# Kernel optimization log

Hardware: AMD Instinct MI355X
Metric: run time of the kernel (lower is better)

## Reference

```python
import jax, jax.numpy as jnp
import numpy as np

D_MODEL = 2048
NUM_HEADS = 16
N_KV_HEADS = 4
HEAD_DIM = D_MODEL // NUM_HEADS  # 128
N_REP = NUM_HEADS // N_KV_HEADS  # 4
WINDOW = 256
ROPE_BASE = 10000.0
B, T = 2, 2048


def setup_inputs() -> dict:
    key = jax.random.key(0)
    ks = jax.random.split(key, 5)
    s_in = 1.0 / np.sqrt(D_MODEL)
    return {
        "x": jax.random.normal(ks[0], (B, T, D_MODEL), jnp.float32),
        "Wq": jax.random.normal(ks[1], (D_MODEL, D_MODEL), jnp.float32) * s_in,
        "Wk": jax.random.normal(ks[2], (D_MODEL, N_KV_HEADS * HEAD_DIM), jnp.float32) * s_in,
        "Wv": jax.random.normal(ks[3], (D_MODEL, N_KV_HEADS * HEAD_DIM), jnp.float32) * s_in,
        "Wo": jax.random.normal(ks[4], (D_MODEL, D_MODEL), jnp.float32) * s_in,
    }


def _rope_tables(seqlen, dtype):
    inv_freq = 1.0 / (ROPE_BASE ** (jnp.arange(0, HEAD_DIM, 2, dtype=jnp.float32) / HEAD_DIM))
    t = jnp.arange(seqlen, dtype=jnp.float32)
    freqs = jnp.outer(t, inv_freq)              # [T, hd/2]
    emb = jnp.concatenate([freqs, freqs], -1)   # [T, hd]
    return jnp.cos(emb).astype(dtype), jnp.sin(emb).astype(dtype)


def _rotate_half(x):
    half = x.shape[-1] // 2
    return jnp.concatenate([-x[..., half:], x[..., :half]], -1)


def reference(x, Wq, Wk, Wv, Wo):
    Bb, Tt, _ = x.shape
    q = (x @ Wq).reshape(Bb, Tt, NUM_HEADS, HEAD_DIM).transpose(0, 2, 1, 3)   # [B,H,T,hd]
    k = (x @ Wk).reshape(Bb, Tt, N_KV_HEADS, HEAD_DIM).transpose(0, 2, 1, 3)  # [B,Hkv,T,hd]
    v = (x @ Wv).reshape(Bb, Tt, N_KV_HEADS, HEAD_DIM).transpose(0, 2, 1, 3)

    cos, sin = _rope_tables(Tt, q.dtype)  # [T, hd] each, broadcast over B,H
    q = q * cos + _rotate_half(q) * sin
    k = k * cos + _rotate_half(k) * sin

    # GQA: repeat kv heads to match query heads
    k = jnp.repeat(k, N_REP, axis=1)
    v = jnp.repeat(v, N_REP, axis=1)

    # banded causal sliding-window mask: 0 <= i - j < WINDOW
    rel = jnp.arange(Tt)[:, None] - jnp.arange(Tt)[None, :]
    allowed = (rel >= 0) & (rel < WINDOW)  # [T, T]

    scale = 1.0 / np.sqrt(HEAD_DIM)
    scores = jnp.einsum('bhqd,bhkd->bhqk', q, k) * scale
    scores = jnp.where(allowed, scores, jnp.finfo(scores.dtype).min)
    probs = jax.nn.softmax(scores, axis=-1)
    y = jnp.einsum('bhqk,bhkd->bhqd', probs, v)
    y = y.transpose(0, 2, 1, 3).reshape(Bb, Tt, D_MODEL)
    return y @ Wo
```

## Files before the change

### kernel.cpp

```cpp
#include <hip/hip_runtime.h>
#include <hip/hip_bf16.h>

#define D_MODEL 2048
#define SEQ_T   2048
#define NQH     16
#define NKVH    4
#define HD      128
#define WIN     256
#define BATCH   2
#define ROWS    (BATCH * SEQ_T)
#define L2_10K  13.287712379549449f
#define GK      2048

typedef __attribute__((ext_vector_type(8))) short bf8_t;
typedef __attribute__((ext_vector_type(4))) float f4_t;

__device__ __forceinline__ float bf2f(unsigned short u) {
    union { unsigned int i; float f; } v; v.i = ((unsigned int)u) << 16; return v.f;
}
__device__ __forceinline__ unsigned short f2bf(float f) {
    union { float f; unsigned int i; } v; v.f = f;
    unsigned int x = v.i;
    unsigned int lsb = (x >> 16) & 1u;
    x += 0x7fffu + lsb;
    return (unsigned short)(x >> 16);
}

__device__ __forceinline__ void async_ld16(const unsigned short* g, unsigned short* l) {
    __builtin_amdgcn_global_load_lds(
        (const __attribute__((address_space(1))) unsigned int*)(g),
        (__attribute__((address_space(3))) unsigned int*)(l), 16, 0, 0);
}

__device__ int sniff_is_f32(const unsigned short* p) {
    int sane = 0;
    for (int i = 0; i < 64; ++i) {
        unsigned short u = p[2 * i];
        int e = (u >> 7) & 0xFF;
        sane += (e >= 100 && e <= 140) ? 1 : 0;
    }
    return sane < 32;
}

__global__ __launch_bounds__(256)
void convert_all(const float* __restrict__ x,
                 const float* __restrict__ Wq, const float* __restrict__ Wk,
                 const float* __restrict__ Wv, const float* __restrict__ Wo,
                 unsigned short* __restrict__ xb,
                 unsigned short* __restrict__ Wqkvt, unsigned short* __restrict__ Wot) {
    __shared__ unsigned short Ts[32][36];
    int id = blockIdx.x;
    const int t = threadIdx.x;
    if (id < 4096) {
        int i = (id * 256 + t) * 8;
        float4 a = *(const float4*)(x + i);
        float4 b = *(const float4*)(x + i + 4);
        ushort4 o0, o1;
        o0.x = f2bf(a.x); o0.y = f2bf(a.y); o0.z = f2bf(a.z); o0.w = f2bf(a.w);
        o1.x = f2bf(b.x); o1.y = f2bf(b.y); o1.z = f2bf(b.z); o1.w = f2bf(b.w);
        *(ushort4*)(xb + i)     = o0;
        *(ushort4*)(xb + i + 4) = o1;
        return;
    }
    id -= 4096;
    const float* W; unsigned short* Wt; int N;
    const int K = D_MODEL;
    if (id < 4096)      { W = Wq; Wt = Wqkvt;                          N = 2048; }
    else if (id < 5120) { W = Wk; Wt = Wqkvt + (size_t)2048 * D_MODEL; N = 512;  id -= 4096; }
    else if (id < 6144) { W = Wv; Wt = Wqkvt + (size_t)2560 * D_MODEL; N = 512;  id -= 5120; }
    else                { W = Wo; Wt = Wot;                            N = 2048; id -= 6144; }
    const int ntn = N >> 5;
    const int n0 = (id % ntn) * 32;
    const int k0 = (id / ntn) * 32;
    {
        int r = t >> 3, c = (t & 7) * 4;
        float4 v = *(const float4*)(W + (size_t)(k0 + r) * N + n0 + c);
        Ts[r][c + 0] = f2bf(v.x); Ts[r][c + 1] = f2bf(v.y);
        Ts[r][c + 2] = f2bf(v.z); Ts[r][c + 3] = f2bf(v.w);
    }
    __syncthreads();
    {
        int n = t >> 3, k = (t & 7) * 4;
        ushort4 o;
        o.x = Ts[k + 0][n]; o.y = Ts[k + 1][n];
        o.z = Ts[k + 2][n]; o.w = Ts[k + 3][n];
        *(ushort4*)(Wt + (size_t)(n0 + n) * K + k0 + k) = o;
    }
}

__global__ __launch_bounds__(256, 3)
void gemm128r(const unsigned short* __restrict__ A,
              const unsigned short* __restrict__ Bt,
              void* __restrict__ Cq, void* __restrict__ Ck, void* __restrict__ Cvc,
              int N, int mode) {
    __shared__ __align__(16) unsigned short Ls[3][8192];

    const int tid  = threadIdx.x;
    const int w    = tid >> 6;
    const int lane = tid & 63;
    const int quad = lane >> 4;
    const int lr   = lane & 15;
    const int wm   = w >> 1;
    const int wn   = w & 1;
    const int sl   = ((quad + (lr >> 1)) & 3) * 8;

    const int ntn = N >> 7;
    const int g   = blockIdx.x;
    const int xcd = g & 7;
    const int r   = g >> 3;
    const int bm  = (xcd & 3) * 8 + (r & 7);
    const int bn  = (xcd >> 2) * (ntn >> 1) + (r >> 3);
    const int m0  = bm * 128;
    const int n0  = bn * 128;

    const unsigned short* srcA[2];
    const unsigned short* srcB[2];
    int dchunk[2];
    #pragma unroll
    for (int l = 0; l < 2; ++l) {
        int li   = l * 256 + tid;
        int row  = li >> 2;
        int slog = ((li & 3) - ((li >> 3) & 3)) & 3;
        srcA[l]   = A  + (size_t)(m0 + row) * GK + slog * 8;
        srcB[l]   = Bt + (size_t)(n0 + row) * GK + slog * 8;
        dchunk[l] = (l * 256 + w * 64) * 8;
    }

    f4_t acc[4][4];
    #pragma unroll
    for (int i = 0; i < 4; ++i)
        #pragma unroll
        for (int j = 0; j < 4; ++j) acc[i][j] = (f4_t){0.f, 0.f, 0.f, 0.f};

#define STAGE(S, KT) do {                                           \
        const int ko_ = (KT) * 32;                                  \
        async_ld16(srcA[0] + ko_, &Ls[S][dchunk[0]]);               \
        async_ld16(srcA[1] + ko_, &Ls[S][dchunk[1]]);               \
        async_ld16(srcB[0] + ko_, &Ls[S][4096 + dchunk[0]]);        \
        async_ld16(srcB[1] + ko_, &Ls[S][4096 + dchunk[1]]);        \
    } while (0)

#define GATE(NN) asm volatile("s_waitcnt vmcnt(" #NN ")" ::: "memory")

    STAGE(0, 0); STAGE(1, 1);
    GATE(4);
    __builtin_amdgcn_s_barrier();

    int Sc = 0, Ss = 2;
    for (int t = 0; t < 64; ++t) {
        const unsigned short* LA = &Ls[Sc][0];
        const unsigned short* LB = &Ls[Sc][4096];
        bf8_t af[4], bv[4];
        #pragma unroll
        for (int mf = 0; mf < 4; ++mf)
            af[mf] = *(const bf8_t*)&LA[(wm * 64 + mf * 16 + lr) * 32 + sl];
        #pragma unroll
        for (int nf = 0; nf < 4; ++nf)
            bv[nf] = *(const bf8_t*)&LB[(wn * 16 + nf * 32 + lr) * 32 + sl];
        if (t < 62) STAGE(Ss, t + 2);
        __builtin_amdgcn_s_setprio(1);
        #pragma unroll
        for (int nf = 0; nf < 4; ++nf)
            #pragma unroll
            for (int mf = 0; mf < 4; ++mf)
                acc[mf][nf] = __builtin_amdgcn_mfma_f32_16x16x32_bf16(
                    af[mf], bv[nf], acc[mf][nf], 0, 0, 0);
        __builtin_amdgcn_s_setprio(0);
        if (t < 62)       GATE(4);
        else if (t == 62) GATE(0);
        if (t < 63) __builtin_amdgcn_s_barrier();
        Sc = (Sc == 2) ? 0 : Sc + 1;
        Ss = (Ss == 2) ? 0 : Ss + 1;
    }

#undef STAGE
#undef GATE

    if (mode == 1) {
        float* C = (float*)Cq;
        #pragma unroll
        for (int mf = 0; mf < 4; ++mf)
            #pragma unroll
            for (int nf = 0; nf < 4; ++nf) {
                int c  = n0 + wn * 16 + nf * 32 + lr;
                int rb = m0 + wm * 64 + mf * 16 + quad * 4;
                #pragma unroll
                for (int rr = 0; rr < 4; ++rr)
                    C[(size_t)(rb + rr) * N + c] = acc[mf][nf][rr];
            }
        return;
    }
    if (n0 < 2048 + 512) {
        const bool isQ = (n0 < 2048);
        unsigned short* Cb = isQ ? (unsigned short*)Cq : (unsigned short*)Ck;
        const int ldc = isQ ? D_MODEL : (NKVH * HD);
        const int cb0 = isQ ? n0 : (n0 - 2048);
        float inv[2];
        #pragma unroll
        for (int p = 0; p < 2; ++p)
            inv[p] = exp2f(-(float)(wn * 16 + p * 32 + lr) * (L2_10K / 64.0f));
        #pragma unroll
        for (int mf = 0; mf < 4; ++mf) {
            #pragma unroll
            for (int rr = 0; rr < 4; ++rr) {
                int row = m0 + wm * 64 + mf * 16 + quad * 4 + rr;
                float tp = (float)(row & (SEQ_T - 1));
                #pragma unroll
                for (int p = 0; p < 2; ++p) {
                    float sn, cs;
                    sincosf(tp * inv[p], &sn, &cs);
                    float lo = acc[mf][p][rr], hi = acc[mf][p + 2][rr];
                    size_t base = (size_t)row * ldc + cb0 + wn * 16 + p * 32 + lr;
                    Cb[base]      = f2bf(lo * cs - hi * sn);
                    Cb[base + 64] = f2bf(hi * cs + lo * sn);
                }
            }
        }
    } else {
        unsigned short* Vc = (unsigned short*)Cvc;
        #pragma unroll
        for (int mf = 0; mf < 4; ++mf)
            #pragma unroll
            for (int nf = 0; nf < 4; ++nf) {
                int n    = (n0 - 2560) + wn * 16 + nf * 32 + lr;
                int kvh2 = n >> 7, d = n & 127;
                int row0 = m0 + wm * 64 + mf * 16 + quad * 4;
                int bb   = row0 >> 11, pos = row0 & (SEQ_T - 1);
                ushort4 o;
                o.x = f2bf(acc[mf][nf][0]); o.y = f2bf(acc[mf][nf][1]);
                o.z = f2bf(acc[mf][nf][2]); o.w = f2bf(acc[mf][nf][3]);
                *(ushort4*)(Vc + (size_t)(bb * 4 + kvh2) * (SEQ_T * HD)
                              + (size_t)(pos >> 5) * 4096 + d * 32 + (pos & 31)) = o;
            }
    }
}

__global__ __launch_bounds__(512, 2)
void gemm128(const unsigned short* __restrict__ A,
             const unsigned short* __restrict__ Bt,
             float* __restrict__ C, int N) {
    __shared__ __align__(16) unsigned short Ls[4][12288];

    const int tid  = threadIdx.x;
    const int w    = tid >> 6;
    const int lane = tid & 63;
    const int quad = lane >> 4;
    const int lr   = lane & 15;
    const int wm   = w >> 2;
    const int wn   = w & 3;
    const int sl   = ((quad + (lr >> 1)) & 3) * 8;

    const int ntn = N >> 8;
    const int g   = blockIdx.x;
    const int xcd = g & 7;
    const int r   = g >> 3;
    const int bm  = (xcd & 3) * 8 + (r & 7);
    const int bn  = (xcd >> 2) * (ntn >> 1) + (r >> 3);
    const int m0  = bm * 128;
    const int n0  = bn * 256;

    const int slog = ((tid & 3) - ((tid >> 3) & 3)) & 3;
    const unsigned short* srcA0 = A  + (size_t)(m0 + (tid >> 2)) * GK + slog * 8;
    const unsigned short* srcB0 = Bt + (size_t)(n0 + (tid >> 2)) * GK + slog * 8;
    const unsigned short* srcB1 = Bt + (size_t)(n0 + 128 + (tid >> 2)) * GK + slog * 8;
    const int dch = w * 512;

    f4_t acc[4][4];
    #pragma unroll
    for (int i = 0; i < 4; ++i)
        #pragma unroll
        for (int j = 0; j < 4; ++j) acc[i][j] = (f4_t){0.f, 0.f, 0.f, 0.f};

#define STAGEB(S, KT) do {                                          \
        const int ko_ = (KT) * 32;                                  \
        async_ld16(srcA0 + ko_, &Ls[S][dch]);                       \
        async_ld16(srcB0 + ko_, &Ls[S][4096 + dch]);                \
        async_ld16(srcB1 + ko_, &Ls[S][8192 + dch]);                \
    } while (0)

#define GATE(NN) asm volatile("s_waitcnt vmcnt(" #NN ")" ::: "memory")

    STAGEB(0, 0); STAGEB(1, 1); STAGEB(2, 2);
    GATE(6);
    __builtin_amdgcn_s_barrier();

    bf8_t af[4], bv[4];
    for (int t = 0; t < 64; ++t) {
        const int S = t & 3;
        #pragma unroll
        for (int mf = 0; mf < 4; ++mf)
            af[mf] = *(const bf8_t*)&Ls[S][(wm * 64 + mf * 16 + lr) * 32 + sl];
        #pragma unroll
        for (int nf = 0; nf < 4; ++nf)
            bv[nf] = *(const bf8_t*)&Ls[S][4096 + (wn * 16 + nf * 64 + lr) * 32 + sl];
        if (t < 61) STAGEB((t + 3) & 3, t + 3);
        __builtin_amdgcn_s_barrier();
        __builtin_amdgcn_s_setprio(1);
        #pragma unroll
        for (int nf = 0; nf < 4; ++nf)
            #pragma unroll
            for (int mf = 0; mf < 4; ++mf)
                acc[mf][nf] = __builtin_amdgcn_mfma_f32_16x16x32_bf16(
                    af[mf], bv[nf], acc[mf][nf], 0, 0, 0);
        __builtin_amdgcn_s_setprio(0);
        if (t < 61)      GATE(6);
        else if (t == 61) GATE(3);
        else if (t == 62) GATE(0);
        if (t < 63) __builtin_amdgcn_s_barrier();
    }

#undef STAGEB
#undef GATE

    #pragma unroll
    for (int mf = 0; mf < 4; ++mf)
        #pragma unroll
        for (int nf = 0; nf < 4; ++nf) {
            int c  = n0 + wn * 16 + nf * 64 + lr;
            int rb = m0 + wm * 64 + mf * 16 + quad * 4;
            #pragma unroll
            for (int rr = 0; rr < 4; ++rr)
                C[(size_t)(rb + rr) * N + c] = acc[mf][nf][rr];
        }
}

__global__ __launch_bounds__(256)
void gemm_dual(const void* __restrict__ A, const void* __restrict__ B,
               void* __restrict__ C, int M, int N, int Kd,
               const unsigned short* __restrict__ sniffp,
               int a_dyn, int c_dyn, int c_trans) {
    __shared__ unsigned short As[64][32];
    __shared__ unsigned short Bs[64][32];
    __shared__ int s_f32;

    const int t = threadIdx.x;
    if (t == 0) s_f32 = sniff_is_f32(sniffp);

    const int m0 = blockIdx.y * 64, n0 = blockIdx.x * 64;
    const int w = t >> 6, lane = t & 63;
    const int wm = w >> 1, wn = w & 1;
    const int quad = lane >> 4, lr = lane & 15;

    f4_t acc[2][2];
    #pragma unroll
    for (int i = 0; i < 2; ++i)
        #pragma unroll
        for (int j = 0; j < 2; ++j)
            acc[i][j] = (f4_t){0.f, 0.f, 0.f, 0.f};

    const int ar = t >> 2, ac = (t & 3) * 8;
    const int bk = t >> 3, bn = (t & 7) * 8;

    __syncthreads();
    const bool in_f32 = (s_f32 != 0);
    const bool a_f32  = in_f32 && (a_dyn != 0);
    const bool c_f32  = in_f32 && (c_dyn != 0);

    for (int k0 = 0; k0 < Kd; k0 += 32) {
        __syncthreads();
        if (a_f32) {
            const float* Af = (const float*)A;
            const float4* pa = (const float4*)(Af + (size_t)(m0 + ar) * Kd + k0 + ac);
            float4 a0 = pa[0], a1 = pa[1];
            unsigned short* d = &As[ar][ac];
            d[0] = f2bf(a0.x); d[1] = f2bf(a0.y); d[2] = f2bf(a0.z); d[3] = f2bf(a0.w);
            d[4] = f2bf(a1.x); d[5] = f2bf(a1.y); d[6] = f2bf(a1.z); d[7] = f2bf(a1.w);
        } else {
            const unsigned short* Au = (const unsigned short*)A;
            *(uint4*)(&As[ar][ac]) = *(const uint4*)(Au + (size_t)(m0 + ar) * Kd + k0 + ac);
        }
        if (in_f32) {
            const float* Bf = (const float*)B;
            const float4* pb = (const float4*)(Bf + (size_t)(k0 + bk) * N + n0 + bn);
            float4 b0 = pb[0], b1 = pb[1];
            Bs[bn + 0][bk] = f2bf(b0.x); Bs[bn + 1][bk] = f2bf(b0.y);
            Bs[bn + 2][bk] = f2bf(b0.z); Bs[bn + 3][bk] = f2bf(b0.w);
            Bs[bn + 4][bk] = f2bf(b1.x); Bs[bn + 5][bk] = f2bf(b1.y);
            Bs[bn + 6][bk] = f2bf(b1.z); Bs[bn + 7][bk] = f2bf(b1.w);
        } else {
            const unsigned short* Bu = (const unsigned short*)B;
            uint4 bv = *(const uint4*)(Bu + (size_t)(k0 + bk) * N + n0 + bn);
            union { uint4 v; unsigned short s[8]; } bu; bu.v = bv;
            #pragma unroll
            for (int j = 0; j < 8; ++j) Bs[bn + j][bk] = bu.s[j];
        }
        __syncthreads();

        bf8_t va0 = *(const bf8_t*)&As[wm * 32 + 0  + lr][quad * 8];
        bf8_t va1 = *(const bf8_t*)&As[wm * 32 + 16 + lr][quad * 8];
        bf8_t vb0 = *(const bf8_t*)&Bs[wn * 32 + 0  + lr][quad * 8];
        bf8_t vb1 = *(const bf8_t*)&Bs[wn * 32 + 16 + lr][quad * 8];

        acc[0][0] = __builtin_amdgcn_mfma_f32_16x16x32_bf16(va0, vb0, acc[0][0], 0, 0, 0);
        acc[0][1] = __builtin_amdgcn_mfma_f32_16x16x32_bf16(va0, vb1, acc[0][1], 0, 0, 0);
        acc[1][0] = __builtin_amdgcn_mfma_f32_16x16x32_bf16(va1, vb0, acc[1][0], 0, 0, 0);
        acc[1][1] = __builtin_amdgcn_mfma_f32_16x16x32_bf16(va1, vb1, acc[1][1], 0, 0, 0);
    }

    if (c_trans) {
        #pragma unroll
        for (int mi = 0; mi < 2; ++mi)
            #pragma unroll
            for (int ni = 0; ni < 2; ++ni) {
                int row0 = m0 + wm * 32 + mi * 16 + quad * 4;
                int col  = n0 + wn * 32 + ni * 16 + lr;
                int kvh2 = col >> 7, d = col & 127;
                int bb   = row0 >> 11, pos = row0 & (SEQ_T - 1);
                ushort4 v;
                v.x = f2bf(acc[mi][ni][0]); v.y = f2bf(acc[mi][ni][1]);
                v.z = f2bf(acc[mi][ni][2]); v.w = f2bf(acc[mi][ni][3]);
                *(ushort4*)((unsigned short*)C + (size_t)(bb * 4 + kvh2) * (SEQ_T * HD)
                              + (size_t)(pos >> 5) * 4096 + d * 32 + (pos & 31)) = v;
            }
    } else {
        #pragma unroll
        for (int mi = 0; mi < 2; ++mi)
            #pragma unroll
            for (int ni = 0; ni < 2; ++ni)
                #pragma unroll
                for (int r = 0; r < 4; ++r) {
                    int row = m0 + wm * 32 + mi * 16 + quad * 4 + r;
                    int col = n0 + wn * 32 + ni * 16 + lr;
                    if (c_f32) ((float*)C)[(size_t)row * N + col] = acc[mi][ni][r];
                    else ((unsigned short*)C)[(size_t)row * N + col] = f2bf(acc[mi][ni][r]);
                }
    }
}

__global__ __launch_bounds__(64)
void rope_kernel(unsigned short* __restrict__ X, int nheads) {
    const int idx = blockIdx.x;
    const int h   = idx % nheads;
    const int row = idx / nheads;
    const int tpos = row % SEQ_T;
    const int i   = threadIdx.x;

    size_t base = (size_t)row * (nheads * HD) + h * HD;
    float inv = exp2f(-(float)i * (L2_10K / 64.0f));
    float a = (float)tpos * inv;
    float s, c;
    sincosf(a, &s, &c);
    float x0 = bf2f(X[base + i]);
    float x1 = bf2f(X[base + i + 64]);
    X[base + i]      = f2bf(x0 * c - x1 * s);
    X[base + i + 64] = f2bf(x1 * c + x0 * s);
}

#define PS  72

__global__ __launch_bounds__(64)
void attn_gqa(unsigned short* __restrict__ Q,
              const unsigned short* __restrict__ K,
              const unsigned short* __restrict__ Vc) {
    __shared__ unsigned short Pw[32][PS];

    const int t    = threadIdx.x;
    const int g    = blockIdx.x;
    const int xcd  = g & 7;
    const int b    = xcd >> 2;
    const int kvh  = xcd & 3;
    const int h4   = (g >> 3) & 3;
    const int q0   = (g >> 5) * 32;
    const int quad = t >> 4;
    const int lr   = t & 15;
    const int h    = kvh * 4 + h4;
    const float scale = 0.08838834764831845f;

    bf8_t qf[2][4];
    #pragma unroll
    for (int mt = 0; mt < 2; ++mt) {
        const unsigned short* qrow =
            Q + (size_t)(b * SEQ_T + q0 + mt * 16 + lr) * D_MODEL + h * HD;
        #pragma unroll
        for (int kk = 0; kk < 4; ++kk)
            qf[mt][kk] = *(const bf8_t*)(qrow + kk * 32 + quad * 8);
    }

    f4_t O[2][8];
    #pragma unroll
    for (int mt = 0; mt < 2; ++mt)
        #pragma unroll
        for (int dt = 0; dt < 8; ++dt) O[mt][dt] = (f4_t){0.f, 0.f, 0.f, 0.f};
    float lpart[2][4];
    #pragma unroll
    for (int mt = 0; mt < 2; ++mt)
        #pragma unroll
        for (int r = 0; r < 4; ++r) lpart[mt][r] = 0.f;

    const size_t vbase = (size_t)(b * 4 + kvh) * (SEQ_T * HD);
    const int jstart = (q0 >= 193) ? 0 : ((193 - q0 + 63) >> 6);

    for (int j = jstart; j < 5; ++j) {
        const int kb = q0 - 256 + 64 * j;
        const bool need_mask = (j == 0) || (j == 4) || (kb < 0);

        bf8_t kf[4][4];
        #pragma unroll
        for (int nt = 0; nt < 4; ++nt) {
            int rg = kb + nt * 16 + lr;
            rg = rg < 0 ? 0 : (rg > SEQ_T - 1 ? SEQ_T - 1 : rg);
            const unsigned short* kr =
                K + (size_t)(b * SEQ_T + rg) * (NKVH * HD) + kvh * HD;
            #pragma unroll
            for (int kk = 0; kk < 4; ++kk)
                kf[nt][kk] = *(const bf8_t*)(kr + kk * 32 + quad * 8);
        }

        f4_t s[2][4];
        #pragma unroll
        for (int mt = 0; mt < 2; ++mt)
            #pragma unroll
            for (int nt = 0; nt < 4; ++nt) s[mt][nt] = (f4_t){0.f, 0.f, 0.f, 0.f};
        #pragma unroll
        for (int nt = 0; nt < 4; ++nt)
            #pragma unroll
            for (int kk = 0; kk < 4; ++kk) {
                s[0][nt] = __builtin_amdgcn_mfma_f32_16x16x32_bf16(qf[0][kk], kf[nt][kk], s[0][nt], 0, 0, 0);
                s[1][nt] = __builtin_amdgcn_mfma_f32_16x16x32_bf16(qf[1][kk], kf[nt][kk], s[1][nt], 0, 0, 0);
            }

        bf8_t vf[2][8];
        #pragma unroll
        for (int kk = 0; kk < 2; ++kk) {
            int slb = (kb + kk * 32) >> 5;
            slb = slb < 0 ? 0 : (slb > 63 ? 63 : slb);
            const unsigned short* vbp = Vc + vbase + (size_t)slb * 4096 + quad * 8;
            #pragma unroll
            for (int dt = 0; dt < 8; ++dt)
                vf[kk][dt] = *(const bf8_t*)(vbp + (dt * 16 + lr) * 32);
        }

        #pragma unroll
        for (int mt = 0; mt < 2; ++mt)
            #pragma unroll
            for (int r = 0; r < 4; ++r) {
                const int q = q0 + mt * 16 + quad * 4 + r;
                #pragma unroll
                for (int nt = 0; nt < 4; ++nt) {
                    float pj = __expf(s[mt][nt][r] * scale);
                    if (need_mask) {
                        int jg = kb + nt * 16 + lr;
                        bool ok = (jg >= 0) && ((unsigned)(q - jg) < (unsigned)WIN);
                        pj = ok ? pj : 0.f;
                    }
                    lpart[mt][r] += pj;
                    Pw[mt * 16 + quad * 4 + r][nt * 16 + lr] = f2bf(pj);
                }
            }

        bf8_t pf[2][2];
        #pragma unroll
        for (int mt = 0; mt < 2; ++mt)
            #pragma unroll
            for (int kk = 0; kk < 2; ++kk)
                pf[mt][kk] = *(const bf8_t*)&Pw[mt * 16 + lr][kk * 32 + quad * 8];
        #pragma unroll
        for (int dt = 0; dt < 8; ++dt)
            #pragma unroll
            for (int kk = 0; kk < 2; ++kk) {
                O[0][dt] = __builtin_amdgcn_mfma_f32_16x16x32_bf16(pf[0][kk], vf[kk][dt], O[0][dt], 0, 0, 0);
                O[1][dt] = __builtin_amdgcn_mfma_f32_16x16x32_bf16(pf[1][kk], vf[kk][dt], O[1][dt], 0, 0, 0);
            }
    }

    #pragma unroll
    for (int off = 1; off < 16; off <<= 1)
        #pragma unroll
        for (int mt = 0; mt < 2; ++mt)
            #pragma unroll
            for (int r = 0; r < 4; ++r)
                lpart[mt][r] += __shfl_xor(lpart[mt][r], off);

    #pragma unroll
    for (int mt = 0; mt < 2; ++mt) {
        float invl[4];
        #pragma unroll
        for (int r = 0; r < 4; ++r) invl[r] = 1.0f / lpart[mt][r];
        #pragma unroll
        for (int dt = 0; dt < 8; ++dt)
            #pragma unroll
            for (int r = 0; r < 4; ++r)
                Q[(size_t)(b * SEQ_T + q0 + mt * 16 + quad * 4 + r) * D_MODEL
                  + h * HD + dt * 16 + lr] = f2bf(O[mt][dt][r] * invl[r]);
    }
}

extern "C" void kernel_launch(void* const* d_in, const int* in_sizes, int n_in,
                              void* d_out, int out_size, void* d_ws, size_t ws_size,
                              hipStream_t stream) {
    const float* x  = (const float*)d_in[0];
    const float* Wq = (const float*)d_in[1];
    const float* Wk = (const float*)d_in[2];
    const float* Wv = (const float*)d_in[3];
    const float* Wo = (const float*)d_in[4];
    const unsigned short* sniffp = (const unsigned short*)d_in[1];

    unsigned short* Qb  = (unsigned short*)d_ws;
    unsigned short* Kb  = Qb + (size_t)ROWS * D_MODEL;
    unsigned short* Vcb = Kb + (size_t)ROWS * (NKVH * HD);
    unsigned short* Wot = Vcb + (size_t)(NKVH * HD) * ROWS;

    dim3 blk(256);

    if (ws_size >= (size_t)32 * 1024 * 1024) {
        unsigned short* xb    = (unsigned short*)d_out;
        unsigned short* Wqkvt = xb + (size_t)ROWS * D_MODEL;

        convert_all<<<dim3(14336), blk, 0, stream>>>(x, Wq, Wk, Wv, Wo, xb, Wqkvt, Wot);

        gemm128r<<<dim3(768), blk, 0, stream>>>(
            xb, Wqkvt, Qb, Kb, Vcb, D_MODEL + 2 * NKVH * HD, 3);

        attn_gqa<<<dim3(2048), dim3(64), 0, stream>>>(Qb, Kb, Vcb);

        gemm128<<<dim3(256), dim3(512), 0, stream>>>(Qb, Wot, (float*)d_out, D_MODEL);
    } else {
        gemm_dual<<<dim3(D_MODEL / 64, ROWS / 64), blk, 0, stream>>>(
            x, Wq, Qb, ROWS, D_MODEL, D_MODEL, sniffp, 1, 0, 0);
        gemm_dual<<<dim3((NKVH * HD) / 64, ROWS / 64), blk, 0, stream>>>(
            x, Wk, Kb, ROWS, NKVH * HD, D_MODEL, sniffp, 1, 0, 0);
        gemm_dual<<<dim3((NKVH * HD) / 64, ROWS / 64), blk, 0, stream>>>(
            x, Wv, Vcb, ROWS, NKVH * HD, D_MODEL, sniffp, 1, 0, 1);
        rope_kernel<<<dim3(ROWS * NQH), dim3(64), 0, stream>>>(Qb, NQH);
        rope_kernel<<<dim3(ROWS * NKVH), dim3(64), 0, stream>>>(Kb, NKVH);
        attn_gqa<<<dim3(2048), dim3(64), 0, stream>>>(Qb, Kb, Vcb);
        gemm_dual<<<dim3(D_MODEL / 64, ROWS / 64), blk, 0, stream>>>(
            Qb, Wo, d_out, ROWS, D_MODEL, D_MODEL, sniffp, 0, 1, 0);
    }
}
```

Before: 253.9 us.

## Share K tile in LDS across two GQA query heads per attention block

The attention kernel now runs two wavefronts per block, each handling a different query head of the same KV group. The K tile is loaded cooperatively into shared memory once and read by both waves, instead of each wave loading it from global memory. V loading is also split per kk to lower register pressure. The cost is two __syncthreads per key block and fewer blocks in flight, in exchange for halving K traffic.

```diff
diff --git a/kernel.cpp b/kernel.cpp
--- a/kernel.cpp
+++ b/kernel.cpp
@@ -446,24 +446,28 @@
     X[base + i + 64] = f2bf(x1 * c + x0 * s);
 }
 
+#define KSS 136
 #define PS  72
 
-__global__ __launch_bounds__(64)
+__global__ __launch_bounds__(128)
 void attn_gqa(unsigned short* __restrict__ Q,
               const unsigned short* __restrict__ K,
               const unsigned short* __restrict__ Vc) {
-    __shared__ unsigned short Pw[32][PS];
+    __shared__ unsigned short Ks[64][KSS];
+    __shared__ unsigned short Pw[2][32][PS];
 
     const int t    = threadIdx.x;
     const int g    = blockIdx.x;
     const int xcd  = g & 7;
     const int b    = xcd >> 2;
     const int kvh  = xcd & 3;
-    const int h4   = (g >> 3) & 3;
-    const int q0   = (g >> 5) * 32;
-    const int quad = t >> 4;
-    const int lr   = t & 15;
-    const int h    = kvh * 4 + h4;
+    const int hp   = (g >> 3) & 1;
+    const int q0   = (g >> 4) * 32;
+    const int w    = t >> 6;
+    const int lane = t & 63;
+    const int quad = lane >> 4;
+    const int lr   = lane & 15;
+    const int h    = kvh * 4 + hp * 2 + w;
     const float scale = 0.08838834764831845f;
 
     bf8_t qf[2][4];
@@ -488,50 +492,42 @@
         for (int r = 0; r < 4; ++r) lpart[mt][r] = 0.f;
 
     const size_t vbase = (size_t)(b * 4 + kvh) * (SEQ_T * HD);
-    const int jstart = (q0 >= 193) ? 0 : ((193 - q0 + 63) >> 6);
-
-    for (int j = jstart; j < 5; ++j) {
+    const int krow = t >> 1, kcol = (t & 1) * 64;
+
+    for (int j = 0; j < 5; ++j) {
         const int kb = q0 - 256 + 64 * j;
+        if (kb + 63 < 0) continue;
         const bool need_mask = (j == 0) || (j == 4) || (kb < 0);
 
-        bf8_t kf[4][4];
+        __syncthreads();
+        {
+            int rg = kb + krow;
+            rg = rg < 0 ? 0 : (rg > SEQ_T - 1 ? SEQ_T - 1 : rg);
+            const unsigned short* src =
+                K + (size_t)(b * SEQ_T + rg) * (NKVH * HD) + kvh * HD + kcol;
+            #pragma unroll
+            for (int i = 0; i < 8; ++i)
+                *(uint4*)&Ks[krow][kcol + 8 * i] = *(const uint4*)(src + 8 * i);
+        }
+        __syncthreads();
+
+        f4_t s[2][4];
+        #pragma unroll
+        for (int mt = 0; mt < 2; ++mt)
+            #pragma unroll
+            for (int nt = 0; nt < 4; ++nt) s[mt][nt] = (f4_t){0.f, 0.f, 0.f, 0.f};
         #pragma unroll
         for (int nt = 0; nt < 4; ++nt) {
-            int rg = kb + nt * 16 + lr;
-            rg = rg < 0 ? 0 : (rg > SEQ_T - 1 ? SEQ_T - 1 : rg);
-            const unsigned short* kr =
-                K + (size_t)(b * SEQ_T + rg) * (NKVH * HD) + kvh * HD;
-            #pragma unroll
-            for (int kk = 0; kk < 4; ++kk)
-                kf[nt][kk] = *(const bf8_t*)(kr + kk * 32 + quad * 8);
-        }
-
-        f4_t s[2][4];
-        #pragma unroll
-        for (int mt = 0; mt < 2; ++mt)
-            #pragma unroll
-            for (int nt = 0; nt < 4; ++nt) s[mt][nt] = (f4_t){0.f, 0.f, 0.f, 0.f};
-        #pragma unroll
-        for (int nt = 0; nt < 4; ++nt)
             #pragma unroll
             for (int kk = 0; kk < 4; ++kk) {
-                s[0][nt] = __builtin_amdgcn_mfma_f32_16x16x32_bf16(qf[0][kk], kf[nt][kk], s[0][nt], 0, 0, 0);
-                s[1][nt] = __builtin_amdgcn_mfma_f32_16x16x32_bf16(qf[1][kk], kf[nt][kk], s[1][nt], 0, 0, 0);
+                bf8_t kf = *(const bf8_t*)&Ks[nt * 16 + lr][kk * 32 + quad * 8];
+                s[0][nt] = __builtin_amdgcn_mfma_f32_16x16x32_bf16(qf[0][kk], kf, s[0][nt], 0, 0, 0);
+                s[1][nt] = __builtin_amdgcn_mfma_f32_16x16x32_bf16(qf[1][kk], kf, s[1][nt], 0, 0, 0);
             }
-
-        bf8_t vf[2][8];
-        #pragma unroll
-        for (int kk = 0; kk < 2; ++kk) {
-            int slb = (kb + kk * 32) >> 5;
-            slb = slb < 0 ? 0 : (slb > 63 ? 63 : slb);
-            const unsigned short* vbp = Vc + vbase + (size_t)slb * 4096 + quad * 8;
-            #pragma unroll
-            for (int dt = 0; dt < 8; ++dt)
-                vf[kk][dt] = *(const bf8_t*)(vbp + (dt * 16 + lr) * 32);
-        }
-
-        #pragma unroll
-        for (int mt = 0; mt < 2; ++mt)
+        }
+
+        #pragma unroll
+        for (int mt = 0; mt < 2; ++mt) {
             #pragma unroll
             for (int r = 0; r < 4; ++r) {
                 const int q = q0 + mt * 16 + quad * 4 + r;
@@ -544,23 +540,32 @@
                         pj = ok ? pj : 0.f;
                     }
                     lpart[mt][r] += pj;
-                    Pw[mt * 16 + quad * 4 + r][nt * 16 + lr] = f2bf(pj);
+                    Pw[w][mt * 16 + quad * 4 + r][nt * 16 + lr] = f2bf(pj);
                 }
             }
+        }
 
         bf8_t pf[2][2];
         #pragma unroll
         for (int mt = 0; mt < 2; ++mt)
             #pragma unroll
             for (int kk = 0; kk < 2; ++kk)
-                pf[mt][kk] = *(const bf8_t*)&Pw[mt * 16 + lr][kk * 32 + quad * 8];
-        #pragma unroll
-        for (int dt = 0; dt < 8; ++dt)
-            #pragma unroll
-            for (int kk = 0; kk < 2; ++kk) {
-                O[0][dt] = __builtin_amdgcn_mfma_f32_16x16x32_bf16(pf[0][kk], vf[kk][dt], O[0][dt], 0, 0, 0);
-                O[1][dt] = __builtin_amdgcn_mfma_f32_16x16x32_bf16(pf[1][kk], vf[kk][dt], O[1][dt], 0, 0, 0);
+                pf[mt][kk] = *(const bf8_t*)&Pw[w][mt * 16 + lr][kk * 32 + quad * 8];
+        #pragma unroll
+        for (int kk = 0; kk < 2; ++kk) {
+            int slb = (kb + kk * 32) >> 5;
+            slb = slb < 0 ? 0 : (slb > 63 ? 63 : slb);
+            const unsigned short* vbp = Vc + vbase + (size_t)slb * 4096 + quad * 8;
+            bf8_t vf[8];
+            #pragma unroll
+            for (int dt = 0; dt < 8; ++dt)
+                vf[dt] = *(const bf8_t*)(vbp + (dt * 16 + lr) * 32);
+            #pragma unroll
+            for (int dt = 0; dt < 8; ++dt) {
+                O[0][dt] = __builtin_amdgcn_mfma_f32_16x16x32_bf16(pf[0][kk], vf[dt], O[0][dt], 0, 0, 0);
+                O[1][dt] = __builtin_amdgcn_mfma_f32_16x16x32_bf16(pf[1][kk], vf[dt], O[1][dt], 0, 0, 0);
             }
+        }
     }
 
     #pragma unroll
@@ -611,7 +616,7 @@
         gemm128r<<<dim3(768), blk, 0, stream>>>(
             xb, Wqkvt, Qb, Kb, Vcb, D_MODEL + 2 * NKVH * HD, 3);
 
-        attn_gqa<<<dim3(2048), dim3(64), 0, stream>>>(Qb, Kb, Vcb);
+        attn_gqa<<<dim3(1024), dim3(128), 0, stream>>>(Qb, Kb, Vcb);
 
         gemm128<<<dim3(256), dim3(512), 0, stream>>>(Qb, Wot, (float*)d_out, D_MODEL);
     } else {
@@ -623,7 +628,7 @@
             x, Wv, Vcb, ROWS, NKVH * HD, D_MODEL, sniffp, 1, 0, 1);
         rope_kernel<<<dim3(ROWS * NQH), dim3(64), 0, stream>>>(Qb, NQH);
         rope_kernel<<<dim3(ROWS * NKVH), dim3(64), 0, stream>>>(Kb, NKVH);
-        attn_gqa<<<dim3(2048), dim3(64), 0, stream>>>(Qb, Kb, Vcb);
+        attn_gqa<<<dim3(1024), dim3(128), 0, stream>>>(Qb, Kb, Vcb);
         gemm_dual<<<dim3(D_MODEL / 64, ROWS / 64), blk, 0, stream>>>(
             Qb, Wo, d_out, ROWS, D_MODEL, D_MODEL, sniffp, 0, 1, 0);
     }
```

After: 246.4 us. -2.9%, faster.
